# Performance work log

Measured on AMD Instinct MI355X. Metric: run time of the kernel, lower is better.

Reference implementation:

```python
import jax, jax.numpy as jnp
import numpy as np

NB_HEAD = 8
SIZE_PER_HEAD = 64
MAX_LEN = 1024
MASK_PENALTY = 1e12


def setup_inputs() -> dict:
    key = jax.random.key(0)
    ks = jax.random.split(key, 6)
    B, L, D_IN = 8, MAX_LEN, 512
    D_OUT = NB_HEAD * SIZE_PER_HEAD
    return {
        "Q_seq": jax.random.normal(ks[0], (B, L, D_IN), dtype=jnp.float32),
        "K_seq": jax.random.normal(ks[1], (B, L, D_IN), dtype=jnp.float32),
        "V_seq": jax.random.normal(ks[2], (B, L, D_IN), dtype=jnp.float32),
        "WQ": jax.random.normal(ks[3], (D_IN, D_OUT), dtype=jnp.float32) * 0.03,
        "WK": jax.random.normal(ks[4], (D_IN, D_OUT), dtype=jnp.float32) * 0.03,
        "WV": jax.random.normal(ks[5], (D_IN, D_OUT), dtype=jnp.float32) * 0.03,
    }


def reference(Q_seq, K_seq, V_seq, WQ, WK, WV):
    B, L, _ = Q_seq.shape
    H, D = NB_HEAD, SIZE_PER_HEAD
    # project and split heads: [B, L, H*D] -> [B, H, L, D]
    q = (Q_seq @ WQ).reshape(B, L, H, D).transpose(0, 2, 1, 3)
    k = (K_seq @ WK).reshape(B, L, H, D).transpose(0, 2, 1, 3)
    v = (V_seq @ WV).reshape(B, L, H, D).transpose(0, 2, 1, 3)
    scale = 1.0 / jnp.sqrt(jnp.asarray(D, dtype=q.dtype))
    scores = jnp.einsum('bhqd,bhkd->bhqk', q, k) * scale  # [B,H,L,L]
    # Mask(): eye+cumsum construction == causal mask (penalize key > query)
    causal = jnp.triu(jnp.ones((L, L), dtype=scores.dtype), k=1)
    scores = scores - causal * MASK_PENALTY
    A = jax.nn.softmax(scores, axis=-1)
    O = jnp.einsum('bhqk,bhkd->bhqd', A, v)  # [B,H,L,D]
    return O.transpose(0, 2, 1, 3).reshape(B, L, H * D)
```

## Files before the change

kernel.cpp:

```cpp
#include <hip/hip_runtime.h>

#define NH 8
#define DH 64
#define SL 1024
#define NB 8
#define DIN 512
#define DOUT 512
#define PS 72

typedef __bf16 bf16x8 __attribute__((ext_vector_type(8)));
typedef float floatx4 __attribute__((ext_vector_type(4)));
typedef unsigned short ushortx8 __attribute__((ext_vector_type(8)));

__device__ __forceinline__ unsigned short f2bf(float f) {
    unsigned int u = __builtin_bit_cast(unsigned int, f);
    u += 0x7FFFu + ((u >> 16) & 1u);
    return (unsigned short)(u >> 16);
}

__device__ __forceinline__ floatx4 mfma_bf16(bf16x8 a, bf16x8 b, floatx4 c) {
    return __builtin_amdgcn_mfma_f32_16x16x32_bf16(a, b, c, 0, 0, 0);
}

__device__ __forceinline__ void gld_lds16(const unsigned short* g, unsigned short* l) {
    __builtin_amdgcn_global_load_lds(
        (const __attribute__((address_space(1))) unsigned int*)g,
        (__attribute__((address_space(3))) unsigned int*)l, 16, 0, 0);
}

__device__ __forceinline__ unsigned int pack_bf2(float a, float b) {
    return __builtin_amdgcn_perm(__builtin_bit_cast(unsigned int, b),
                                 __builtin_bit_cast(unsigned int, a), 0x07060302u);
}

__global__ __launch_bounds__(256) void prep_kernel(const float* __restrict__ Qs,
                                                   const float* __restrict__ Ks,
                                                   const float* __restrict__ Vs,
                                                   const float* __restrict__ WQ,
                                                   const float* __restrict__ WK,
                                                   const float* __restrict__ WV,
                                                   unsigned short* __restrict__ xb,
                                                   unsigned short* __restrict__ wt) {
    __shared__ unsigned short tile[64][68];
    const int bid = blockIdx.x;
    if (bid < 6144) {
        const int z = bid >> 11;
        const float* X = (z == 0) ? Qs : (z == 1 ? Ks : Vs);
        const int t = (bid & 2047) * 256 + threadIdx.x;
        const int row = t >> 6, c = t & 63;
        const float4 a = *(const float4*)(X + t * 8);
        const float4 b = *(const float4*)(X + t * 8 + 4);
        ushortx8 o;
        o[0] = f2bf(a.x); o[1] = f2bf(a.y); o[2] = f2bf(a.z); o[3] = f2bf(a.w);
        o[4] = f2bf(b.x); o[5] = f2bf(b.y); o[6] = f2bf(b.z); o[7] = f2bf(b.w);
        const int dst = (((row >> 7) * 8 + (c >> 3)) * 128 + (row & 127)) * 64 +
                        (((c & 7) ^ (row & 7)) * 8);
        *(ushortx8*)(xb + z * 8192 * DIN + dst) = o;
    } else {
        const int b2 = bid - 6144;
        const int z = b2 >> 6;
        const int r = b2 & 63;
        const float* W = (z == 0) ? WQ : (z == 1 ? WK : WV);
        const int k0 = (r >> 3) * 64, n0 = (r & 7) * 64;
        const int tn = threadIdx.x & 63, tk = threadIdx.x >> 6;
#pragma unroll
        for (int i = 0; i < 16; ++i) {
            const int kk = tk + i * 4;
            tile[tn][kk] = f2bf(W[(k0 + kk) * DOUT + n0 + tn]);
        }
        __syncthreads();
#pragma unroll
        for (int i = 0; i < 16; ++i) {
            const int nn = tk + i * 4;
            const int n = n0 + nn, k = k0 + tn;
            const int dst = (((z * 4 + (n >> 7)) * 8 + (k >> 6)) * 128 + (n & 127)) * 64 +
                            ((((k >> 3) & 7) ^ (n & 7)) * 8) + (k & 7);
            wt[dst] = tile[nn][tn];
        }
    }
}

__global__ __launch_bounds__(256) void proj_kernel(const unsigned short* __restrict__ xbt,
                                                   const unsigned short* __restrict__ wtt,
                                                   unsigned short* __restrict__ qw,
                                                   unsigned short* __restrict__ ks,
                                                   unsigned short* __restrict__ vs) {
    __shared__ __align__(16) unsigned short S[16384];
    unsigned short* As = S;
    unsigned short* Bs = S + 8192;
    const int z = blockIdx.y;
    const int wg = blockIdx.x;
    const int ix = wg >> 3;
    const int mblk = (wg & 7) * 8 + (ix >> 2);
    const int nblk = ix & 3;
    const int w = threadIdx.x >> 6, lane = threadIdx.x & 63;
    const int l15 = lane & 15, quad = lane >> 4;
    const int wm = w >> 1, wn = w & 1;
    const int soff = lane * 8;
    const unsigned short* Ab = xbt + z * (8192 * DIN) + mblk * 8 * 8192 + (w * 4) * 512 + soff;
    const unsigned short* Bb = wtt + (z * 4 + nblk) * 8 * 8192 + (w * 4) * 512 + soff;
    unsigned short* Asw = &As[(w * 4) * 512];
    unsigned short* Bsw = &Bs[(w * 4) * 512];

    floatx4 acc[4][4];
#pragma unroll
    for (int i = 0; i < 4; ++i)
#pragma unroll
        for (int j = 0; j < 4; ++j) acc[i][j] = floatx4{0.f, 0.f, 0.f, 0.f};

    for (int kblk = 0; kblk < 8; ++kblk) {
        __syncthreads();
#pragma unroll
        for (int i = 0; i < 4; ++i) {
            gld_lds16(Ab + kblk * 8192 + i * 512, Asw + i * 512);
            gld_lds16(Bb + kblk * 8192 + i * 512, Bsw + i * 512);
        }
        __syncthreads();
#pragma unroll
        for (int ksub = 0; ksub < 2; ++ksub) {
            bf16x8 af[4], bfr[4];
#pragma unroll
            for (int mi = 0; mi < 4; ++mi) {
                const int row = wm * 64 + mi * 16 + l15;
                af[mi] = *(const bf16x8*)&As[row * 64 + (((quad + ksub * 4) ^ (l15 & 7)) * 8)];
            }
#pragma unroll
            for (int nt = 0; nt < 4; ++nt) {
                const int row = wn * 64 + nt * 16 + l15;
                bfr[nt] = *(const bf16x8*)&Bs[row * 64 + (((quad + ksub * 4) ^ (l15 & 7)) * 8)];
            }
#pragma unroll
            for (int mi = 0; mi < 4; ++mi)
#pragma unroll
                for (int nt = 0; nt < 4; ++nt)
                    acc[mi][nt] = mfma_bf16(af[mi], bfr[nt], acc[mi][nt]);
        }
    }

    __syncthreads();
#pragma unroll
    for (int mi = 0; mi < 4; ++mi)
#pragma unroll
        for (int nt = 0; nt < 4; ++nt)
#pragma unroll
            for (int r = 0; r < 4; ++r) {
                const int a = wm * 64 + mi * 16 + quad * 4 + r;
                const int c = wn * 64 + nt * 16 + l15;
                const int h = c >> 6, dh = c & 63;
                float v = acc[mi][nt][r];
                int lidx;
                if (z == 0) {
                    v *= 0.18033688f;
                    lidx = h * 8192 + (a >> 4) * 1024 + (dh >> 3) * 128 + (a & 15) * 8 + (dh & 7);
                } else if (z == 1) {
                    lidx = (((((h << 3) + (a >> 4)) << 1) | (dh >> 5))) * 512 +
                           (a & 15) * 32 + (dh & 31);
                } else {
                    const int s64 = ((a & 15) << 2) | ((a >> 4) & 3);
                    lidx = ((((h << 1) | (a >> 6)) << 1) | (s64 >> 5)) * 2048 +
                           dh * 32 + (s64 & 31);
                }
                S[lidx] = f2bf(v);
            }
    __syncthreads();

    const int b = mblk >> 3;
    const int li0 = (mblk & 7) * 128;
    const int tid = threadIdx.x;
    unsigned short* outp = (z == 0) ? qw : (z == 1 ? ks : vs);
#pragma unroll
    for (int j = 0; j < 8; ++j) {
        const int off = j * 2048 + tid * 8;
        const ushortx8 val = *(const ushortx8*)(S + off);
        int gidx;
        if (z == 0) {
            const int h = off >> 13, o13 = off & 8191;
            gidx = ((b * 8 + nblk * 2 + h) * 64 + (li0 >> 4) + (o13 >> 10)) * 1024 + (o13 & 1023);
        } else if (z == 1) {
            const int region = off >> 9, pos = off & 511;
            const int h = region >> 4, g = (region >> 1) & 7, d5 = region & 1;
            gidx = (((b * 8 + nblk * 2 + h) * 64 + (li0 >> 4) + g) * 2 + d5) * 512 + pos;
        } else {
            const int region = off >> 11, pos = off & 2047;
            const int h = region >> 2, l6 = (region >> 1) & 1, s5 = region & 1;
            gidx = ((b * 8 + nblk * 2 + h) * 32 + (li0 >> 5) + l6 * 2 + s5) * 2048 + pos;
        }
        *(ushortx8*)(outp + gidx) = val;
    }
}

__global__ __launch_bounds__(256) void attn_kernel(const unsigned short* __restrict__ qw,
                                                   const unsigned short* __restrict__ ksp,
                                                   const unsigned short* __restrict__ vsp,
                                                   float* __restrict__ out) {
    __shared__ union {
        unsigned short Ps[4][16 * PS];
        float Cb[2][64][21];
    } sh;
    const int w = threadIdx.x >> 6;
    const int lane = threadIdx.x & 63;
    const int l15 = lane & 15, quad = lane >> 4;
    const int s_ = blockIdx.x;
    const int xcd = s_ & 7;
    const int idx = s_ >> 3;
    const int bh = xcd * 8 + (idx & 7);
    const int xblk = idx >> 3;
    const int b = bh >> 3, h = bh & 7;
    const int tile = (w < 2) ? xblk : 63 - xblk;
    const int half = w & 1;
    const int m0 = tile * 16;

    const unsigned short* qp = qw + (bh * 64 + tile) * 1024 + quad * 128 + l15 * 8;
    const bf16x8 aQ0 = *(const bf16x8*)qp;
    const bf16x8 aQ1 = *(const bf16x8*)(qp + 512);

    const unsigned short* ksb = ksp + (bh * 64) * 2 * 512 + l15 * 32 + quad * 8;
    const unsigned short* vsb = vsp + (bh * 32 * 64 + l15) * 32 + quad * 8;
    unsigned short* myPs = sh.Ps[w];

    float lrow[4] = {0.f, 0.f, 0.f, 0.f};
    floatx4 o0 = {0.f, 0.f, 0.f, 0.f}, o1 = o0, o2 = o0, o3 = o0;
    const floatx4 zf = {0.f, 0.f, 0.f, 0.f};

    auto TAIL = [&](int kt, floatx4* s, bool domask, const bf16x8* v0, const bf16x8* v1) {
#pragma unroll
        for (int r = 0; r < 4; ++r) {
            const int row = m0 + quad * 4 + r;
            float p[4];
#pragma unroll
            for (int t = 0; t < 4; ++t) {
                float e = __builtin_amdgcn_exp2f(s[t][r]);
                if (domask && (kt + t * 16 + l15 > row)) e = 0.f;
                p[t] = e;
            }
            lrow[r] += (p[0] + p[1]) + (p[2] + p[3]);
            uint2 pk;
            pk.x = pack_bf2(p[0], p[1]);
            pk.y = pack_bf2(p[2], p[3]);
            *(uint2*)(myPs + (quad * 4 + r) * PS + l15 * 4) = pk;
        }
        __builtin_amdgcn_wave_barrier();
        const bf16x8 aP0 = *(const bf16x8*)(myPs + l15 * PS + quad * 8);
        const bf16x8 aP1 = *(const bf16x8*)(myPs + l15 * PS + 32 + quad * 8);
        __builtin_amdgcn_wave_barrier();
        __builtin_amdgcn_s_setprio(1);
        o0 = mfma_bf16(aP1, v1[0], mfma_bf16(aP0, v0[0], o0));
        o1 = mfma_bf16(aP1, v1[1], mfma_bf16(aP0, v0[1], o1));
        o2 = mfma_bf16(aP1, v1[2], mfma_bf16(aP0, v0[2], o2));
        o3 = mfma_bf16(aP1, v1[3], mfma_bf16(aP0, v0[3], o3));
        __builtin_amdgcn_s_setprio(0);
    };

    auto BODY = [&](int kt) {
        const unsigned short* kp = ksb + (kt >> 4) * 1024;
        floatx4 s[4];
        __builtin_amdgcn_s_setprio(1);
#pragma unroll
        for (int t = 0; t < 4; ++t) {
            const bf16x8 k0 = *(const bf16x8*)(kp + t * 1024);
            const bf16x8 k1 = *(const bf16x8*)(kp + t * 1024 + 512);
            s[t] = mfma_bf16(aQ1, k1, mfma_bf16(aQ0, k0, zf));
        }
        __builtin_amdgcn_s_setprio(0);
        const unsigned short* vb = vsb + (kt >> 5) * 2048;
        bf16x8 v0[4], v1[4];
#pragma unroll
        for (int dt = 0; dt < 4; ++dt) {
            v0[dt] = *(const bf16x8*)(vb + dt * 512);
            v1[dt] = *(const bf16x8*)(vb + dt * 512 + 2048);
        }
        TAIL(kt, s, false, v0, v1);
    };

    auto BODYM = [&](int kt) {
        const unsigned short* kp = ksb + (kt >> 4) * 1024;
        floatx4 s[4] = {zf, zf, zf, zf};
        __builtin_amdgcn_s_setprio(1);
#pragma unroll
        for (int t = 0; t < 4; ++t) {
            if (kt + t * 16 <= m0 + 15) {
                const bf16x8 k0 = *(const bf16x8*)(kp + t * 1024);
                const bf16x8 k1 = *(const bf16x8*)(kp + t * 1024 + 512);
                s[t] = mfma_bf16(aQ1, k1, mfma_bf16(aQ0, k0, zf));
            }
        }
        __builtin_amdgcn_s_setprio(0);
        const unsigned short* vb = vsb + (kt >> 5) * 2048;
        bf16x8 v0[4], v1[4];
#pragma unroll
        for (int dt = 0; dt < 4; ++dt) {
            v0[dt] = *(const bf16x8*)(vb + dt * 512);
            v1[dt] = *(const bf16x8*)(vb + dt * 512 + 2048);
        }
        TAIL(kt, s, true, v0, v1);
    };

    const int nf = (tile + 4) >> 2;
    const int last = nf - 1;
    for (int j = half; j < last; j += 2) BODY(j * 64);
    if ((last & 1) == half) BODYM(last * 64);

    __syncthreads();
    if (half == 1) {
        float* cb = &sh.Cb[w >> 1][lane][0];
#pragma unroll
        for (int r = 0; r < 4; ++r) {
            cb[r] = o0[r]; cb[4 + r] = o1[r];
            cb[8 + r] = o2[r]; cb[12 + r] = o3[r];
            cb[16 + r] = lrow[r];
        }
    }
    __syncthreads();
    if (half == 0) {
        const float* cb = &sh.Cb[w >> 1][lane][0];
#pragma unroll
        for (int r = 0; r < 4; ++r) {
            o0[r] += cb[r]; o1[r] += cb[4 + r];
            o2[r] += cb[8 + r]; o3[r] += cb[12 + r];
            lrow[r] += cb[16 + r];
        }
#pragma unroll
        for (int r = 0; r < 4; ++r) {
            float l = lrow[r];
            l += __shfl_xor(l, 1);
            l += __shfl_xor(l, 2);
            l += __shfl_xor(l, 4);
            l += __shfl_xor(l, 8);
            const float inv = 1.0f / l;
            const int row = m0 + quad * 4 + r;
            float* op = out + (b * SL + row) * DOUT + h * DH + l15;
            op[0]  = o0[r] * inv;
            op[16] = o1[r] * inv;
            op[32] = o2[r] * inv;
            op[48] = o3[r] * inv;
        }
    }
}

extern "C" void kernel_launch(void* const* d_in, const int* in_sizes, int n_in,
                              void* d_out, int out_size, void* d_ws, size_t ws_size,
                              hipStream_t stream) {
    const float* Qs = (const float*)d_in[0];
    const float* Ks = (const float*)d_in[1];
    const float* Vs = (const float*)d_in[2];
    const float* WQ = (const float*)d_in[3];
    const float* WK = (const float*)d_in[4];
    const float* WV = (const float*)d_in[5];
    float* out = (float*)d_out;

    unsigned short* xb = (unsigned short*)d_ws;
    unsigned short* wt = xb + 3 * 8192 * DIN;
    unsigned short* qw = wt + 3 * DIN * DOUT;
    unsigned short* ks = qw + NB * NH * SL * DH;
    unsigned short* vs = ks + NB * NH * SL * DH;

    prep_kernel<<<dim3(6336), 256, 0, stream>>>(Qs, Ks, Vs, WQ, WK, WV, xb, wt);
    proj_kernel<<<dim3(256, 3), 256, 0, stream>>>(xb, wt, qw, ks, vs);
    attn_kernel<<<dim3(2048), 256, 0, stream>>>(qw, ks, vs, out);
}
```

Measured before the change: 164.0 us.

## Process two 16-row query tiles per wave to reuse K/V fragments

Each wave now handles 32 query rows, as two 16-row sub-tiles, instead of 16. Every K and V fragment loaded from global memory then feeds twice as many MFMAs. The attention grid is halved to 1024 blocks, and the causal pairing of tiles is now done over 32-row groups. In exchange, register use and LDS use per wave go up, and there are fewer blocks to hide latency and balance load across CUs.

Result: faster. 158.2 us (-3.5%).

```diff
diff --git a/kernel.cpp b/kernel.cpp
--- a/kernel.cpp
+++ b/kernel.cpp
@@ -194,8 +194,8 @@
                                                    const unsigned short* __restrict__ vsp,
                                                    float* __restrict__ out) {
     __shared__ union {
-        unsigned short Ps[4][16 * PS];
-        float Cb[2][64][21];
+        unsigned short Ps[4][32 * PS];
+        float Cb[2][64][42];
     } sh;
     const int w = threadIdx.x >> 6;
     const int lane = threadIdx.x & 63;
@@ -204,62 +204,79 @@
     const int xcd = s_ & 7;
     const int idx = s_ >> 3;
     const int bh = xcd * 8 + (idx & 7);
-    const int xblk = idx >> 3;
+    const int xb16 = idx >> 3;
     const int b = bh >> 3, h = bh & 7;
-    const int tile = (w < 2) ? xblk : 63 - xblk;
+    const int p = (w < 2) ? xb16 : 31 - xb16;
     const int half = w & 1;
-    const int m0 = tile * 16;
-
-    const unsigned short* qp = qw + (bh * 64 + tile) * 1024 + quad * 128 + l15 * 8;
-    const bf16x8 aQ0 = *(const bf16x8*)qp;
-    const bf16x8 aQ1 = *(const bf16x8*)(qp + 512);
+    const int m0 = p * 32;
+
+    const unsigned short* qpA = qw + (bh * 64 + 2 * p) * 1024 + quad * 128 + l15 * 8;
+    const bf16x8 aQA0 = *(const bf16x8*)qpA;
+    const bf16x8 aQA1 = *(const bf16x8*)(qpA + 512);
+    const bf16x8 aQB0 = *(const bf16x8*)(qpA + 1024);
+    const bf16x8 aQB1 = *(const bf16x8*)(qpA + 1536);
 
     const unsigned short* ksb = ksp + (bh * 64) * 2 * 512 + l15 * 32 + quad * 8;
     const unsigned short* vsb = vsp + (bh * 32 * 64 + l15) * 32 + quad * 8;
     unsigned short* myPs = sh.Ps[w];
 
-    float lrow[4] = {0.f, 0.f, 0.f, 0.f};
-    floatx4 o0 = {0.f, 0.f, 0.f, 0.f}, o1 = o0, o2 = o0, o3 = o0;
+    float lrowA[4] = {0.f, 0.f, 0.f, 0.f};
+    float lrowB[4] = {0.f, 0.f, 0.f, 0.f};
+    floatx4 oA[4], oB[4];
     const floatx4 zf = {0.f, 0.f, 0.f, 0.f};
-
-    auto TAIL = [&](int kt, floatx4* s, bool domask, const bf16x8* v0, const bf16x8* v1) {
+#pragma unroll
+    for (int dt = 0; dt < 4; ++dt) { oA[dt] = zf; oB[dt] = zf; }
+
+    auto TAIL = [&](int kt, floatx4* sA, floatx4* sB, bool domask,
+                    const bf16x8* v0, const bf16x8* v1) {
 #pragma unroll
         for (int r = 0; r < 4; ++r) {
-            const int row = m0 + quad * 4 + r;
-            float p[4];
+            const int rowA = m0 + quad * 4 + r;
+            float pa[4], pb[4];
 #pragma unroll
             for (int t = 0; t < 4; ++t) {
-                float e = __builtin_amdgcn_exp2f(s[t][r]);
-                if (domask && (kt + t * 16 + l15 > row)) e = 0.f;
-                p[t] = e;
-            }
-            lrow[r] += (p[0] + p[1]) + (p[2] + p[3]);
-            uint2 pk;
-            pk.x = pack_bf2(p[0], p[1]);
-            pk.y = pack_bf2(p[2], p[3]);
-            *(uint2*)(myPs + (quad * 4 + r) * PS + l15 * 4) = pk;
+                float ea = __builtin_amdgcn_exp2f(sA[t][r]);
+                float eb = __builtin_amdgcn_exp2f(sB[t][r]);
+                if (domask) {
+                    const int key = kt + t * 16 + l15;
+                    if (key > rowA) ea = 0.f;
+                    if (key > rowA + 16) eb = 0.f;
+                }
+                pa[t] = ea; pb[t] = eb;
+            }
+            lrowA[r] += (pa[0] + pa[1]) + (pa[2] + pa[3]);
+            lrowB[r] += (pb[0] + pb[1]) + (pb[2] + pb[3]);
+            uint2 pkA, pkB;
+            pkA.x = pack_bf2(pa[0], pa[1]); pkA.y = pack_bf2(pa[2], pa[3]);
+            pkB.x = pack_bf2(pb[0], pb[1]); pkB.y = pack_bf2(pb[2], pb[3]);
+            *(uint2*)(myPs + (quad * 4 + r) * PS + l15 * 4) = pkA;
+            *(uint2*)(myPs + (16 + quad * 4 + r) * PS + l15 * 4) = pkB;
         }
         __builtin_amdgcn_wave_barrier();
-        const bf16x8 aP0 = *(const bf16x8*)(myPs + l15 * PS + quad * 8);
-        const bf16x8 aP1 = *(const bf16x8*)(myPs + l15 * PS + 32 + quad * 8);
+        const bf16x8 aPA0 = *(const bf16x8*)(myPs + l15 * PS + quad * 8);
+        const bf16x8 aPA1 = *(const bf16x8*)(myPs + l15 * PS + 32 + quad * 8);
+        const bf16x8 aPB0 = *(const bf16x8*)(myPs + (16 + l15) * PS + quad * 8);
+        const bf16x8 aPB1 = *(const bf16x8*)(myPs + (16 + l15) * PS + 32 + quad * 8);
         __builtin_amdgcn_wave_barrier();
         __builtin_amdgcn_s_setprio(1);
-        o0 = mfma_bf16(aP1, v1[0], mfma_bf16(aP0, v0[0], o0));
-        o1 = mfma_bf16(aP1, v1[1], mfma_bf16(aP0, v0[1], o1));
-        o2 = mfma_bf16(aP1, v1[2], mfma_bf16(aP0, v0[2], o2));
-        o3 = mfma_bf16(aP1, v1[3], mfma_bf16(aP0, v0[3], o3));
+#pragma unroll
+        for (int dt = 0; dt < 4; ++dt) {
+            oA[dt] = mfma_bf16(aPA1, v1[dt], mfma_bf16(aPA0, v0[dt], oA[dt]));
+            oB[dt] = mfma_bf16(aPB1, v1[dt], mfma_bf16(aPB0, v0[dt], oB[dt]));
+        }
         __builtin_amdgcn_s_setprio(0);
     };
 
     auto BODY = [&](int kt) {
         const unsigned short* kp = ksb + (kt >> 4) * 1024;
-        floatx4 s[4];
+        floatx4 sA[4], sB[4];
         __builtin_amdgcn_s_setprio(1);
 #pragma unroll
         for (int t = 0; t < 4; ++t) {
             const bf16x8 k0 = *(const bf16x8*)(kp + t * 1024);
             const bf16x8 k1 = *(const bf16x8*)(kp + t * 1024 + 512);
-            s[t] = mfma_bf16(aQ1, k1, mfma_bf16(aQ0, k0, zf));
+            sA[t] = mfma_bf16(aQA1, k1, mfma_bf16(aQA0, k0, zf));
+            sB[t] = mfma_bf16(aQB1, k1, mfma_bf16(aQB0, k0, zf));
         }
         __builtin_amdgcn_s_setprio(0);
         const unsigned short* vb = vsb + (kt >> 5) * 2048;
@@ -269,19 +286,23 @@
             v0[dt] = *(const bf16x8*)(vb + dt * 512);
             v1[dt] = *(const bf16x8*)(vb + dt * 512 + 2048);
         }
-        TAIL(kt, s, false, v0, v1);
+        TAIL(kt, sA, sB, false, v0, v1);
     };
 
     auto BODYM = [&](int kt) {
         const unsigned short* kp = ksb + (kt >> 4) * 1024;
-        floatx4 s[4] = {zf, zf, zf, zf};
+        floatx4 sA[4], sB[4];
+#pragma unroll
+        for (int t = 0; t < 4; ++t) { sA[t] = zf; sB[t] = zf; }
         __builtin_amdgcn_s_setprio(1);
 #pragma unroll
         for (int t = 0; t < 4; ++t) {
-            if (kt + t * 16 <= m0 + 15) {
+            if (kt + t * 16 <= m0 + 31) {
                 const bf16x8 k0 = *(const bf16x8*)(kp + t * 1024);
                 const bf16x8 k1 = *(const bf16x8*)(kp + t * 1024 + 512);
-                s[t] = mfma_bf16(aQ1, k1, mfma_bf16(aQ0, k0, zf));
+                if (kt + t * 16 <= m0 + 15)
+                    sA[t] = mfma_bf16(aQA1, k1, mfma_bf16(aQA0, k0, zf));
+                sB[t] = mfma_bf16(aQB1, k1, mfma_bf16(aQB0, k0, zf));
             }
         }
         __builtin_amdgcn_s_setprio(0);
@@ -292,10 +313,10 @@
             v0[dt] = *(const bf16x8*)(vb + dt * 512);
             v1[dt] = *(const bf16x8*)(vb + dt * 512 + 2048);
         }
-        TAIL(kt, s, true, v0, v1);
+        TAIL(kt, sA, sB, true, v0, v1);
     };
 
-    const int nf = (tile + 4) >> 2;
+    const int nf = (m0 + 95) >> 6;
     const int last = nf - 1;
     for (int j = half; j < last; j += 2) BODY(j * 64);
     if ((last & 1) == half) BODYM(last * 64);
@@ -304,35 +325,53 @@
     if (half == 1) {
         float* cb = &sh.Cb[w >> 1][lane][0];
 #pragma unroll
+        for (int dt = 0; dt < 4; ++dt)
+#pragma unroll
+            for (int r = 0; r < 4; ++r) {
+                cb[dt * 4 + r] = oA[dt][r];
+                cb[16 + dt * 4 + r] = oB[dt][r];
+            }
+#pragma unroll
         for (int r = 0; r < 4; ++r) {
-            cb[r] = o0[r]; cb[4 + r] = o1[r];
-            cb[8 + r] = o2[r]; cb[12 + r] = o3[r];
-            cb[16 + r] = lrow[r];
+            cb[32 + r] = lrowA[r];
+            cb[36 + r] = lrowB[r];
         }
     }
     __syncthreads();
     if (half == 0) {
         const float* cb = &sh.Cb[w >> 1][lane][0];
 #pragma unroll
+        for (int dt = 0; dt < 4; ++dt)
+#pragma unroll
+            for (int r = 0; r < 4; ++r) {
+                oA[dt][r] += cb[dt * 4 + r];
+                oB[dt][r] += cb[16 + dt * 4 + r];
+            }
+#pragma unroll
         for (int r = 0; r < 4; ++r) {
-            o0[r] += cb[r]; o1[r] += cb[4 + r];
-            o2[r] += cb[8 + r]; o3[r] += cb[12 + r];
-            lrow[r] += cb[16 + r];
+            lrowA[r] += cb[32 + r];
+            lrowB[r] += cb[36 + r];
         }
 #pragma unroll
         for (int r = 0; r < 4; ++r) {
-            float l = lrow[r];
-            l += __shfl_xor(l, 1);
-            l += __shfl_xor(l, 2);
-            l += __shfl_xor(l, 4);
-            l += __shfl_xor(l, 8);
-            const float inv = 1.0f / l;
-            const int row = m0 + quad * 4 + r;
-            float* op = out + (b * SL + row) * DOUT + h * DH + l15;
-            op[0]  = o0[r] * inv;
-            op[16] = o1[r] * inv;
-            op[32] = o2[r] * inv;
-            op[48] = o3[r] * inv;
+            float lA = lrowA[r], lB = lrowB[r];
+            lA += __shfl_xor(lA, 1); lB += __shfl_xor(lB, 1);
+            lA += __shfl_xor(lA, 2); lB += __shfl_xor(lB, 2);
+            lA += __shfl_xor(lA, 4); lB += __shfl_xor(lB, 4);
+            lA += __shfl_xor(lA, 8); lB += __shfl_xor(lB, 8);
+            const float invA = 1.0f / lA;
+            const float invB = 1.0f / lB;
+            const int rowA = m0 + quad * 4 + r;
+            float* opA = out + (b * SL + rowA) * DOUT + h * DH + l15;
+            float* opB = out + (b * SL + rowA + 16) * DOUT + h * DH + l15;
+            opA[0]  = oA[0][r] * invA;
+            opA[16] = oA[1][r] * invA;
+            opA[32] = oA[2][r] * invA;
+            opA[48] = oA[3][r] * invA;
+            opB[0]  = oB[0][r] * invB;
+            opB[16] = oB[1][r] * invB;
+            opB[32] = oB[2][r] * invB;
+            opB[48] = oB[3][r] * invB;
         }
     }
 }
@@ -356,5 +395,5 @@
 
     prep_kernel<<<dim3(6336), 256, 0, stream>>>(Qs, Ks, Vs, WQ, WK, WV, xb, wt);
     proj_kernel<<<dim3(256, 3), 256, 0, stream>>>(xb, wt, qw, ks, vs);
-    attn_kernel<<<dim3(2048), 256, 0, stream>>>(qw, ks, vs, out);
-}
+    attn_kernel<<<dim3(1024), 256, 0, stream>>>(qw, ks, vs, out);
+}
```

## Process two 16-row query tiles per wave to reuse K/V loads

Applied to the files above, without the earlier changes.

Each wave now handles a 32-row query block (two 16-row sub-tiles) instead of one, so every K and V fragment loaded from global memory feeds twice as many MFMAs. The grid is halved to 1024 blocks, and shared-memory P staging and the cross-wave combine buffer are doubled. The aim is to cut redundant global K/V traffic per unit of work. In exchange it uses more registers and LDS, and having fewer blocks may reduce occupancy and worsen load balance across CUs.

Measured after the change: 158.3 us. -3.5%, faster.

```diff
diff --git a/kernel.cpp b/kernel.cpp
--- a/kernel.cpp
+++ b/kernel.cpp
@@ -189,13 +189,106 @@
     }
 }
 
+template <bool DOMASK>
+__device__ __forceinline__ void frame_step(
+    int kt, int m0, int l15, int quad,
+    const unsigned short* __restrict__ ksb,
+    const unsigned short* __restrict__ vsb,
+    unsigned short* myPs,
+    bf16x8 aQA0, bf16x8 aQA1, bf16x8 aQB0, bf16x8 aQB1,
+    floatx4& oA0, floatx4& oA1, floatx4& oA2, floatx4& oA3,
+    floatx4& oB0, floatx4& oB1, floatx4& oB2, floatx4& oB3,
+    float& lA0, float& lA1, float& lA2, float& lA3,
+    float& lB0, float& lB1, float& lB2, float& lB3) {
+    const floatx4 zf = {0.f, 0.f, 0.f, 0.f};
+    const unsigned short* kp = ksb + (kt >> 4) * 1024;
+    floatx4 sA0 = zf, sA1 = zf, sA2 = zf, sA3 = zf;
+    floatx4 sB0 = zf, sB1 = zf, sB2 = zf, sB3 = zf;
+    __builtin_amdgcn_s_setprio(1);
+#define QK_T(T, SA, SB)                                                     \
+    if (!DOMASK || (kt + T * 16 <= m0 + 31)) {                              \
+        const bf16x8 k0_ = *(const bf16x8*)(kp + T * 1024);                 \
+        const bf16x8 k1_ = *(const bf16x8*)(kp + T * 1024 + 512);           \
+        if (!DOMASK || (kt + T * 16 <= m0 + 15))                            \
+            SA = mfma_bf16(aQA1, k1_, mfma_bf16(aQA0, k0_, zf));            \
+        SB = mfma_bf16(aQB1, k1_, mfma_bf16(aQB0, k0_, zf));                \
+    }
+    QK_T(0, sA0, sB0)
+    QK_T(1, sA1, sB1)
+    QK_T(2, sA2, sB2)
+    QK_T(3, sA3, sB3)
+#undef QK_T
+    __builtin_amdgcn_s_setprio(0);
+    const unsigned short* vb = vsb + (kt >> 5) * 2048;
+    const bf16x8 v00 = *(const bf16x8*)(vb);
+    const bf16x8 v01 = *(const bf16x8*)(vb + 512);
+    const bf16x8 v02 = *(const bf16x8*)(vb + 1024);
+    const bf16x8 v03 = *(const bf16x8*)(vb + 1536);
+    const bf16x8 v10 = *(const bf16x8*)(vb + 2048);
+    const bf16x8 v11 = *(const bf16x8*)(vb + 2560);
+    const bf16x8 v12 = *(const bf16x8*)(vb + 3072);
+    const bf16x8 v13 = *(const bf16x8*)(vb + 3584);
+#define TAIL_R(R, LA, LB)                                                    \
+    {                                                                        \
+        const int rowA = m0 + quad * 4 + R;                                  \
+        float pa0 = __builtin_amdgcn_exp2f(sA0[R]);                          \
+        float pa1 = __builtin_amdgcn_exp2f(sA1[R]);                          \
+        float pa2 = __builtin_amdgcn_exp2f(sA2[R]);                          \
+        float pa3 = __builtin_amdgcn_exp2f(sA3[R]);                          \
+        float pb0 = __builtin_amdgcn_exp2f(sB0[R]);                          \
+        float pb1 = __builtin_amdgcn_exp2f(sB1[R]);                          \
+        float pb2 = __builtin_amdgcn_exp2f(sB2[R]);                          \
+        float pb3 = __builtin_amdgcn_exp2f(sB3[R]);                          \
+        if (DOMASK) {                                                        \
+            if (kt + l15 > rowA) pa0 = 0.f;                                  \
+            if (kt + 16 + l15 > rowA) pa1 = 0.f;                             \
+            if (kt + 32 + l15 > rowA) pa2 = 0.f;                             \
+            if (kt + 48 + l15 > rowA) pa3 = 0.f;                             \
+            if (kt + l15 > rowA + 16) pb0 = 0.f;                             \
+            if (kt + 16 + l15 > rowA + 16) pb1 = 0.f;                        \
+            if (kt + 32 + l15 > rowA + 16) pb2 = 0.f;                        \
+            if (kt + 48 + l15 > rowA + 16) pb3 = 0.f;                        \
+        }                                                                    \
+        LA += (pa0 + pa1) + (pa2 + pa3);                                     \
+        LB += (pb0 + pb1) + (pb2 + pb3);                                     \
+        uint2 pkA, pkB;                                                      \
+        pkA.x = pack_bf2(pa0, pa1);                                          \
+        pkA.y = pack_bf2(pa2, pa3);                                          \
+        pkB.x = pack_bf2(pb0, pb1);                                          \
+        pkB.y = pack_bf2(pb2, pb3);                                          \
+        *(uint2*)(myPs + (quad * 4 + R) * PS + l15 * 4) = pkA;               \
+        *(uint2*)(myPs + (16 + quad * 4 + R) * PS + l15 * 4) = pkB;          \
+    }
+    TAIL_R(0, lA0, lB0)
+    TAIL_R(1, lA1, lB1)
+    TAIL_R(2, lA2, lB2)
+    TAIL_R(3, lA3, lB3)
+#undef TAIL_R
+    __builtin_amdgcn_wave_barrier();
+    const bf16x8 aPA0 = *(const bf16x8*)(myPs + l15 * PS + quad * 8);
+    const bf16x8 aPA1 = *(const bf16x8*)(myPs + l15 * PS + 32 + quad * 8);
+    const bf16x8 aPB0 = *(const bf16x8*)(myPs + (16 + l15) * PS + quad * 8);
+    const bf16x8 aPB1 = *(const bf16x8*)(myPs + (16 + l15) * PS + 32 + quad * 8);
+    __builtin_amdgcn_wave_barrier();
+    __builtin_amdgcn_s_setprio(1);
+    oA0 = mfma_bf16(aPA1, v10, mfma_bf16(aPA0, v00, oA0));
+    oA1 = mfma_bf16(aPA1, v11, mfma_bf16(aPA0, v01, oA1));
+    oA2 = mfma_bf16(aPA1, v12, mfma_bf16(aPA0, v02, oA2));
+    oA3 = mfma_bf16(aPA1, v13, mfma_bf16(aPA0, v03, oA3));
+    oB0 = mfma_bf16(aPB1, v10, mfma_bf16(aPB0, v00, oB0));
+    oB1 = mfma_bf16(aPB1, v11, mfma_bf16(aPB0, v01, oB1));
+    oB2 = mfma_bf16(aPB1, v12, mfma_bf16(aPB0, v02, oB2));
+    oB3 = mfma_bf16(aPB1, v13, mfma_bf16(aPB0, v03, oB3));
+    __builtin_amdgcn_s_setprio(0);
+}
+
 __global__ __launch_bounds__(256) void attn_kernel(const unsigned short* __restrict__ qw,
                                                    const unsigned short* __restrict__ ksp,
                                                    const unsigned short* __restrict__ vsp,
                                                    float* __restrict__ out) {
     __shared__ union {
-        unsigned short Ps[4][16 * PS];
-        float Cb[2][64][21];
+        unsigned short Ps[4][32 * PS];
+        float Cb[2][64][42];
     } sh;
     const int w = threadIdx.x >> 6;
     const int lane = threadIdx.x & 63;
@@ -204,136 +297,90 @@
     const int xcd = s_ & 7;
     const int idx = s_ >> 3;
     const int bh = xcd * 8 + (idx & 7);
-    const int xblk = idx >> 3;
+    const int xb16 = idx >> 3;
     const int b = bh >> 3, h = bh & 7;
-    const int tile = (w < 2) ? xblk : 63 - xblk;
+    const int p = (w < 2) ? xb16 : 31 - xb16;
     const int half = w & 1;
-    const int m0 = tile * 16;
-
-    const unsigned short* qp = qw + (bh * 64 + tile) * 1024 + quad * 128 + l15 * 8;
-    const bf16x8 aQ0 = *(const bf16x8*)qp;
-    const bf16x8 aQ1 = *(const bf16x8*)(qp + 512);
+    const int m0 = p * 32;
+
+    const unsigned short* qpA = qw + (bh * 64 + 2 * p) * 1024 + quad * 128 + l15 * 8;
+    const bf16x8 aQA0 = *(const bf16x8*)qpA;
+    const bf16x8 aQA1 = *(const bf16x8*)(qpA + 512);
+    const bf16x8 aQB0 = *(const bf16x8*)(qpA + 1024);
+    const bf16x8 aQB1 = *(const bf16x8*)(qpA + 1536);
 
     const unsigned short* ksb = ksp + (bh * 64) * 2 * 512 + l15 * 32 + quad * 8;
     const unsigned short* vsb = vsp + (bh * 32 * 64 + l15) * 32 + quad * 8;
     unsigned short* myPs = sh.Ps[w];
 
-    float lrow[4] = {0.f, 0.f, 0.f, 0.f};
-    floatx4 o0 = {0.f, 0.f, 0.f, 0.f}, o1 = o0, o2 = o0, o3 = o0;
     const floatx4 zf = {0.f, 0.f, 0.f, 0.f};
-
-    auto TAIL = [&](int kt, floatx4* s, bool domask, const bf16x8* v0, const bf16x8* v1) {
-#pragma unroll
-        for (int r = 0; r < 4; ++r) {
-            const int row = m0 + quad * 4 + r;
-            float p[4];
-#pragma unroll
-            for (int t = 0; t < 4; ++t) {
-                float e = __builtin_amdgcn_exp2f(s[t][r]);
-                if (domask && (kt + t * 16 + l15 > row)) e = 0.f;
-                p[t] = e;
-            }
-            lrow[r] += (p[0] + p[1]) + (p[2] + p[3]);
-            uint2 pk;
-            pk.x = pack_bf2(p[0], p[1]);
-            pk.y = pack_bf2(p[2], p[3]);
-            *(uint2*)(myPs + (quad * 4 + r) * PS + l15 * 4) = pk;
-        }
-        __builtin_amdgcn_wave_barrier();
-        const bf16x8 aP0 = *(const bf16x8*)(myPs + l15 * PS + quad * 8);
-        const bf16x8 aP1 = *(const bf16x8*)(myPs + l15 * PS + 32 + quad * 8);
-        __builtin_amdgcn_wave_barrier();
-        __builtin_amdgcn_s_setprio(1);
-        o0 = mfma_bf16(aP1, v1[0], mfma_bf16(aP0, v0[0], o0));
-        o1 = mfma_bf16(aP1, v1[1], mfma_bf16(aP0, v0[1], o1));
-        o2 = mfma_bf16(aP1, v1[2], mfma_bf16(aP0, v0[2], o2));
-        o3 = mfma_bf16(aP1, v1[3], mfma_bf16(aP0, v0[3], o3));
-        __builtin_amdgcn_s_setprio(0);
-    };
-
-    auto BODY = [&](int kt) {
-        const unsigned short* kp = ksb + (kt >> 4) * 1024;
-        floatx4 s[4];
-        __builtin_amdgcn_s_setprio(1);
-#pragma unroll
-        for (int t = 0; t < 4; ++t) {
-            const bf16x8 k0 = *(const bf16x8*)(kp + t * 1024);
-            const bf16x8 k1 = *(const bf16x8*)(kp + t * 1024 + 512);
-            s[t] = mfma_bf16(aQ1, k1, mfma_bf16(aQ0, k0, zf));
-        }
-        __builtin_amdgcn_s_setprio(0);
-        const unsigned short* vb = vsb + (kt >> 5) * 2048;
-        bf16x8 v0[4], v1[4];
-#pragma unroll
-        for (int dt = 0; dt < 4; ++dt) {
-            v0[dt] = *(const bf16x8*)(vb + dt * 512);
-            v1[dt] = *(const bf16x8*)(vb + dt * 512 + 2048);
-        }
-        TAIL(kt, s, false, v0, v1);
-    };
-
-    auto BODYM = [&](int kt) {
-        const unsigned short* kp = ksb + (kt >> 4) * 1024;
-        floatx4 s[4] = {zf, zf, zf, zf};
-        __builtin_amdgcn_s_setprio(1);
-#pragma unroll
-        for (int t = 0; t < 4; ++t) {
-            if (kt + t * 16 <= m0 + 15) {
-                const bf16x8 k0 = *(const bf16x8*)(kp + t * 1024);
-                const bf16x8 k1 = *(const bf16x8*)(kp + t * 1024 + 512);
-                s[t] = mfma_bf16(aQ1, k1, mfma_bf16(aQ0, k0, zf));
-            }
-        }
-        __builtin_amdgcn_s_setprio(0);
-        const unsigned short* vb = vsb + (kt >> 5) * 2048;
-        bf16x8 v0[4], v1[4];
-#pragma unroll
-        for (int dt = 0; dt < 4; ++dt) {
-            v0[dt] = *(const bf16x8*)(vb + dt * 512);
-            v1[dt] = *(const bf16x8*)(vb + dt * 512 + 2048);
-        }
-        TAIL(kt, s, true, v0, v1);
-    };
-
-    const int nf = (tile + 4) >> 2;
+    floatx4 oA0 = zf, oA1 = zf, oA2 = zf, oA3 = zf;
+    floatx4 oB0 = zf, oB1 = zf, oB2 = zf, oB3 = zf;
+    float lA0 = 0.f, lA1 = 0.f, lA2 = 0.f, lA3 = 0.f;
+    float lB0 = 0.f, lB1 = 0.f, lB2 = 0.f, lB3 = 0.f;
+
+    const int nf = (m0 + 95) >> 6;
     const int last = nf - 1;
-    for (int j = half; j < last; j += 2) BODY(j * 64);
-    if ((last & 1) == half) BODYM(last * 64);
+    for (int j = half; j < last; j += 2)
+        frame_step<false>(j * 64, m0, l15, quad, ksb, vsb, myPs,
+                          aQA0, aQA1, aQB0, aQB1,
+                          oA0, oA1, oA2, oA3, oB0, oB1, oB2, oB3,
+                          lA0, lA1, lA2, lA3, lB0, lB1, lB2, lB3);
+    if ((last & 1) == half)
+        frame_step<true>(last * 64, m0, l15, quad, ksb, vsb, myPs,
+                         aQA0, aQA1, aQB0, aQB1,
+                         oA0, oA1, oA2, oA3, oB0, oB1, oB2, oB3,
+                         lA0, lA1, lA2, lA3, lB0, lB1, lB2, lB3);
 
     __syncthreads();
     if (half == 1) {
         float* cb = &sh.Cb[w >> 1][lane][0];
-#pragma unroll
-        for (int r = 0; r < 4; ++r) {
-            cb[r] = o0[r]; cb[4 + r] = o1[r];
-            cb[8 + r] = o2[r]; cb[12 + r] = o3[r];
-            cb[16 + r] = lrow[r];
-        }
+        cb[0] = oA0[0];  cb[1] = oA0[1];  cb[2] = oA0[2];  cb[3] = oA0[3];
+        cb[4] = oA1[0];  cb[5] = oA1[1];  cb[6] = oA1[2];  cb[7] = oA1[3];
+        cb[8] = oA2[0];  cb[9] = oA2[1];  cb[10] = oA2[2]; cb[11] = oA2[3];
+        cb[12] = oA3[0]; cb[13] = oA3[1]; cb[14] = oA3[2]; cb[15] = oA3[3];
+        cb[16] = oB0[0]; cb[17] = oB0[1]; cb[18] = oB0[2]; cb[19] = oB0[3];
+        cb[20] = oB1[0]; cb[21] = oB1[1]; cb[22] = oB1[2]; cb[23] = oB1[3];
+        cb[24] = oB2[0]; cb[25] = oB2[1]; cb[26] = oB2[2]; cb[27] = oB2[3];
+        cb[28] = oB3[0]; cb[29] = oB3[1]; cb[30] = oB3[2]; cb[31] = oB3[3];
+        cb[32] = lA0; cb[33] = lA1; cb[34] = lA2; cb[35] = lA3;
+        cb[36] = lB0; cb[37] = lB1; cb[38] = lB2; cb[39] = lB3;
     }
     __syncthreads();
     if (half == 0) {
         const float* cb = &sh.Cb[w >> 1][lane][0];
-#pragma unroll
-        for (int r = 0; r < 4; ++r) {
-            o0[r] += cb[r]; o1[r] += cb[4 + r];
-            o2[r] += cb[8 + r]; o3[r] += cb[12 + r];
-            lrow[r] += cb[16 + r];
-        }
-#pragma unroll
-        for (int r = 0; r < 4; ++r) {
-            float l = lrow[r];
-            l += __shfl_xor(l, 1);
-            l += __shfl_xor(l, 2);
-            l += __shfl_xor(l, 4);
-            l += __shfl_xor(l, 8);
-            const float inv = 1.0f / l;
-            const int row = m0 + quad * 4 + r;
-            float* op = out + (b * SL + row) * DOUT + h * DH + l15;
-            op[0]  = o0[r] * inv;
-            op[16] = o1[r] * inv;
-            op[32] = o2[r] * inv;
-            op[48] = o3[r] * inv;
-        }
+        oA0[0] += cb[0];  oA0[1] += cb[1];  oA0[2] += cb[2];  oA0[3] += cb[3];
+        oA1[0] += cb[4];  oA1[1] += cb[5];  oA1[2] += cb[6];  oA1[3] += cb[7];
+        oA2[0] += cb[8];  oA2[1] += cb[9];  oA2[2] += cb[10]; oA2[3] += cb[11];
+        oA3[0] += cb[12]; oA3[1] += cb[13]; oA3[2] += cb[14]; oA3[3] += cb[15];
+        oB0[0] += cb[16]; oB0[1] += cb[17]; oB0[2] += cb[18]; oB0[3] += cb[19];
+        oB1[0] += cb[20]; oB1[1] += cb[21]; oB1[2] += cb[22]; oB1[3] += cb[23];
+        oB2[0] += cb[24]; oB2[1] += cb[25]; oB2[2] += cb[26]; oB2[3] += cb[27];
+        oB3[0] += cb[28]; oB3[1] += cb[29]; oB3[2] += cb[30]; oB3[3] += cb[31];
+        lA0 += cb[32]; lA1 += cb[33]; lA2 += cb[34]; lA3 += cb[35];
+        lB0 += cb[36]; lB1 += cb[37]; lB2 += cb[38]; lB3 += cb[39];
+#define OUT_R(R, LA, LB)                                                      \
+    {                                                                         \
+        float lAr = LA, lBr = LB;                                             \
+        lAr += __shfl_xor(lAr, 1); lBr += __shfl_xor(lBr, 1);                 \
+        lAr += __shfl_xor(lAr, 2); lBr += __shfl_xor(lBr, 2);                 \
+        lAr += __shfl_xor(lAr, 4); lBr += __shfl_xor(lBr, 4);                 \
+        lAr += __shfl_xor(lAr, 8); lBr += __shfl_xor(lBr, 8);                 \
+        const float invA = 1.0f / lAr;                                        \
+        const float invB = 1.0f / lBr;                                        \
+        const int rowA = m0 + quad * 4 + R;                                   \
+        float* opA = out + (b * SL + rowA) * DOUT + h * DH + l15;             \
+        float* opB = opA + 16 * DOUT;                                         \
+        opA[0] = oA0[R] * invA;  opA[16] = oA1[R] * invA;                     \
+        opA[32] = oA2[R] * invA; opA[48] = oA3[R] * invA;                     \
+        opB[0] = oB0[R] * invB;  opB[16] = oB1[R] * invB;                     \
+        opB[32] = oB2[R] * invB; opB[48] = oB3[R] * invB;                     \
+    }
+        OUT_R(0, lA0, lB0)
+        OUT_R(1, lA1, lB1)
+        OUT_R(2, lA2, lB2)
+        OUT_R(3, lA3, lB3)
+#undef OUT_R
     }
 }
 
@@ -356,5 +403,5 @@
 
     prep_kernel<<<dim3(6336), 256, 0, stream>>>(Qs, Ks, Vs, WQ, WK, WV, xb, wt);
     proj_kernel<<<dim3(256, 3), 256, 0, stream>>>(xb, wt, qw, ks, vs);
-    attn_kernel<<<dim3(2048), 256, 0, stream>>>(qw, ks, vs, out);
-}
+    attn_kernel<<<dim3(1024), 256, 0, stream>>>(qw, ks, vs, out);
+}
```
